# Performance work log

Hardware: AMD Instinct MI355X
Metric: run time of the kernel (lower is better)

The kernel has to match this reference:

```python
import jax, jax.numpy as jnp
import numpy as np

N = 1_000_000   # number of scattered items
D = 256         # in_embed_dim == key_proj_dim
E = 100_000     # nr_elements (number of segments)


def setup_inputs() -> dict:
    key = jax.random.key(0)
    k1, k2, k3, k4, k5 = jax.random.split(key, 5)
    bound = 1.0 / np.sqrt(D)
    scattered_values = jax.random.normal(k1, (N, D), dtype=jnp.float32)
    indices = jax.random.randint(k2, (N,), 0, E, dtype=jnp.int32)
    # key projection Linear(D, D) params (PyTorch default-style init)
    W_key = jax.random.uniform(k3, (D, D), minval=-bound, maxval=bound, dtype=jnp.float32)
    b_key = jax.random.uniform(k4, (D,), minval=-bound, maxval=bound, dtype=jnp.float32)
    # general_attention_weight ~ U(-1/sqrt(key_proj_dim), +)
    attn_w = jax.random.uniform(k5, (D,), minval=-bound, maxval=bound, dtype=jnp.float32)
    return {
        "scattered_values": scattered_values,
        "indices": indices,
        "nr_elements": E,
        "W_key": W_key,
        "b_key": b_key,
        "attn_w": attn_w,
    }


def reference(scattered_values, indices, nr_elements, W_key, b_key, attn_w):
    # key projection: [N, D]
    keys = scattered_values @ W_key.T + b_key
    # general attention logits, scaled: [N]
    probs = (keys @ attn_w) * (D ** -0.5)
    # scatter_softmax over segments (stable: subtract per-segment max)
    seg_max = jax.ops.segment_max(probs, indices, num_segments=nr_elements)
    seg_max = jnp.where(jnp.isfinite(seg_max), seg_max, 0.0)  # empty segments
    ex = jnp.exp(probs - seg_max[indices])
    denom = jax.ops.segment_sum(ex, indices, num_segments=nr_elements)
    scores = ex / denom[indices]
    # weighted scatter-sum of (unprojected) values: [E, D]
    attn_applied = jax.ops.segment_sum(
        scattered_values * scores[:, None], indices, num_segments=nr_elements
    )
    return scores, attn_applied
```

## Files before the change

kernel.cpp:

```cpp
#include <hip/hip_runtime.h>


#define DIM 256
#define WAVE 64

typedef float f4 __attribute__((ext_vector_type(4)));

__global__ void cw_rank_kernel(const float* __restrict__ W,
                               const float* __restrict__ b,
                               const float* __restrict__ a,
                               float* __restrict__ wc,
                               const int* __restrict__ idx,
                               int* __restrict__ counts,
                               int* __restrict__ rank, int n) {
    const int t = threadIdx.x;
    if (blockIdx.x <= DIM) {
        const int k = blockIdx.x;
        __shared__ float sm[256];
        sm[t] = (k < DIM) ? a[t] * W[t * DIM + k] : a[t] * b[t];
        __syncthreads();
        for (int d = 128; d; d >>= 1) {
            if (t < d) sm[t] += sm[t + d];
            __syncthreads();
        }
        if (t == 0) wc[k] = sm[0];
    } else {
        const int i = (blockIdx.x - DIM - 1) * 256 + t;
        if (i < n) rank[i] = atomicAdd(&counts[idx[i]], 1);
    }
}

__global__ void scan1_kernel(const int* __restrict__ counts,
                             int* __restrict__ offsets,
                             int* __restrict__ bsums, int e) {
    __shared__ int s[256];
    const int t = threadIdx.x, g = blockIdx.x * 256 + t;
    const int x = (g < e) ? counts[g] : 0;
    s[t] = x; __syncthreads();
    for (int d = 1; d < 256; d <<= 1) {
        const int v = (t >= d) ? s[t - d] : 0; __syncthreads();
        s[t] += v; __syncthreads();
    }
    if (g < e) offsets[g] = s[t] - x;
    if (t == 255) bsums[blockIdx.x] = s[255];
}

__global__ void scan2_kernel(int* __restrict__ bsums, int nb) {
    __shared__ int s[512];
    const int t = threadIdx.x;
    const int x = (t < nb) ? bsums[t] : 0;
    s[t] = x; __syncthreads();
    for (int d = 1; d < 512; d <<= 1) {
        const int v = (t >= d) ? s[t - d] : 0; __syncthreads();
        s[t] += v; __syncthreads();
    }
    if (t < nb) bsums[t] = s[t] - x;
}

__global__ void scan3_kernel(int* __restrict__ offsets,
                             const int* __restrict__ bsums, int e, int n) {
    const int g = blockIdx.x * 256 + threadIdx.x;
    if (g < e) offsets[g] += bsums[blockIdx.x];
    if (g == 0) offsets[e] = n;
}

__global__ void scatter_kernel(const int* __restrict__ idx,
                               const int* __restrict__ rank,
                               const int* __restrict__ offsets,
                               int* __restrict__ perm, int n) {
    const int i = blockIdx.x * 256 + threadIdx.x;
    if (i < n) perm[offsets[idx[i]] + rank[i]] = i;
}

__global__ void seg_fused_kernel(const f4* __restrict__ v4,
                                 const int* __restrict__ perm,
                                 const float* __restrict__ wc,
                                 const int* __restrict__ offsets,
                                 float* __restrict__ scores,
                                 float* __restrict__ attn, int e) {
    const int lane = threadIdx.x & (WAVE - 1);
    const int s = (blockIdx.x * blockDim.x + threadIdx.x) >> 6;
    if (s >= e) return;
    const f4 wf = ((const f4*)wc)[lane];
    const float c = wc[DIM];
    const int base = offsets[s];
    const int cnt  = offsets[s + 1] - base;
    f4 acc = {0.f, 0.f, 0.f, 0.f};

    if (cnt > 0 && cnt <= WAVE) {
        const int i_l = (lane < cnt) ? perm[base + lane] : 0;
        float myp = 0.f, d = 0.f;
        const int nch = (cnt + 7) >> 3;
        f4 cur[8], nxt[8];
        #pragma unroll
        for (int t = 0; t < 8; ++t)
            if (t < cnt)
                cur[t] = __builtin_nontemporal_load(
                    v4 + (size_t)__shfl(i_l, t, WAVE) * (DIM / 4) + lane);
        for (int ch = 0; ch < nch; ++ch) {
            const int st = ch * 8;
            if (ch + 1 < nch) {
                const int st2 = st + 8;
                #pragma unroll
                for (int t = 0; t < 8; ++t)
                    if (st2 + t < cnt)
                        nxt[t] = __builtin_nontemporal_load(
                            v4 + (size_t)__shfl(i_l, st2 + t, WAVE) * (DIM / 4) + lane);
            }
            #pragma unroll
            for (int t = 0; t < 8; ++t) {
                if (st + t < cnt) {
                    float pp = cur[t].x * wf.x + cur[t].y * wf.y
                             + cur[t].z * wf.z + cur[t].w * wf.w;
                    #pragma unroll
                    for (int off = 32; off; off >>= 1)
                        pp += __shfl_xor(pp, off, WAVE);
                    const float pe = __expf((pp + c) * 0.0625f);
                    d += pe;
                    acc.x += pe * cur[t].x; acc.y += pe * cur[t].y;
                    acc.z += pe * cur[t].z; acc.w += pe * cur[t].w;
                    if (lane == st + t) myp = pe;
                }
            }
            #pragma unroll
            for (int t = 0; t < 8; ++t) cur[t] = nxt[t];
        }
        const float inv = 1.f / d;
        if (lane < cnt) scores[i_l] = myp * inv;
        acc.x *= inv; acc.y *= inv; acc.z *= inv; acc.w *= inv;
    } else if (cnt > WAVE) {
        float d = 0.f;
        for (int t = 0; t < cnt; ++t) {
            const int i = perm[base + t];
            const f4 vv = v4[(size_t)i * (DIM / 4) + lane];
            float pp = vv.x * wf.x + vv.y * wf.y + vv.z * wf.z + vv.w * wf.w;
            #pragma unroll
            for (int off = 32; off; off >>= 1) pp += __shfl_xor(pp, off, WAVE);
            const float pe = __expf((pp + c) * 0.0625f);
            d += pe;
            acc.x += pe * vv.x; acc.y += pe * vv.y;
            acc.z += pe * vv.z; acc.w += pe * vv.w;
        }
        const float inv = 1.f / d;
        for (int t = 0; t < cnt; ++t) {
            const int i = perm[base + t];
            const f4 vv = v4[(size_t)i * (DIM / 4) + lane];
            float pp = vv.x * wf.x + vv.y * wf.y + vv.z * wf.z + vv.w * wf.w;
            #pragma unroll
            for (int off = 32; off; off >>= 1) pp += __shfl_xor(pp, off, WAVE);
            if (lane == 0) scores[i] = __expf((pp + c) * 0.0625f) * inv;
        }
        acc.x *= inv; acc.y *= inv; acc.z *= inv; acc.w *= inv;
    }
    __builtin_nontemporal_store(acc, (f4*)(attn + (size_t)s * DIM) + lane);
}

extern "C" void kernel_launch(void* const* d_in, const int* in_sizes, int n_in,
                              void* d_out, int out_size, void* d_ws, size_t ws_size,
                              hipStream_t stream) {
    const float* v   = (const float*)d_in[0];
    const int*   idx = (const int*)d_in[1];
    const float* W   = (const float*)d_in[3];
    const float* b   = (const float*)d_in[4];
    const float* a   = (const float*)d_in[5];

    const int n = in_sizes[0] / DIM;
    const int e = (out_size - n) / DIM;
    const int nb = (e + 255) / 256;

    float* scores = (float*)d_out;
    float* attn   = (float*)d_out + n;

    float* wc      = (float*)d_ws;
    int*   counts  = (int*)(wc + 512);
    int*   offsets = counts + e;
    int*   bsums   = offsets + e + 2;
    int*   rank    = bsums + 512;
    int*   perm    = rank + n;

    hipMemsetAsync(counts, 0, (size_t)e * sizeof(int), stream);
    cw_rank_kernel<<<DIM + 1 + (n + 255) / 256, 256, 0, stream>>>(
        W, b, a, wc, idx, counts, rank, n);
    scan1_kernel<<<nb, 256, 0, stream>>>(counts, offsets, bsums, e);
    scan2_kernel<<<1, 512, 0, stream>>>(bsums, nb);
    scan3_kernel<<<nb, 256, 0, stream>>>(offsets, bsums, e, n);
    scatter_kernel<<<(n + 255) / 256, 256, 0, stream>>>(idx, rank, offsets, perm, n);

    seg_fused_kernel<<<(e + 3) / 4, 256, 0, stream>>>((const f4*)v, perm, wc,
                                                      offsets, scores, attn, e);
}
```

Before: 284.1 us.

## Replace three-kernel scan with single-pass decoupled look-back scan

Merges the three prefix-scan kernels into one kernel. Each block publishes its aggregate and inclusive prefix through 64-bit status words and looks back at its predecessors using atomics. This removes two kernel launches and the global round trips through the block-sum buffer, so less time goes to launch overhead. In exchange it depends on blocks being scheduled roughly in order and can spin-wait. The status array is zeroed by extending the existing memset.

```diff
diff --git a/kernel.cpp b/kernel.cpp
--- a/kernel.cpp
+++ b/kernel.cpp
@@ -30,38 +30,45 @@
     }
 }
 
-__global__ void scan1_kernel(const int* __restrict__ counts,
-                             int* __restrict__ offsets,
-                             int* __restrict__ bsums, int e) {
+__global__ void scan_lb_kernel(const int* __restrict__ counts,
+                               int* __restrict__ offsets,
+                               unsigned long long* __restrict__ states,
+                               int e, int n) {
     __shared__ int s[256];
-    const int t = threadIdx.x, g = blockIdx.x * 256 + t;
+    __shared__ int px_sm;
+    const int c = blockIdx.x, t = threadIdx.x, g = c * 256 + t;
     const int x = (g < e) ? counts[g] : 0;
     s[t] = x; __syncthreads();
     for (int d = 1; d < 256; d <<= 1) {
         const int v = (t >= d) ? s[t - d] : 0; __syncthreads();
         s[t] += v; __syncthreads();
     }
-    if (g < e) offsets[g] = s[t] - x;
-    if (t == 255) bsums[blockIdx.x] = s[255];
-}
-
-__global__ void scan2_kernel(int* __restrict__ bsums, int nb) {
-    __shared__ int s[512];
-    const int t = threadIdx.x;
-    const int x = (t < nb) ? bsums[t] : 0;
-    s[t] = x; __syncthreads();
-    for (int d = 1; d < 512; d <<= 1) {
-        const int v = (t >= d) ? s[t - d] : 0; __syncthreads();
-        s[t] += v; __syncthreads();
+    const int A = s[255];
+    if (t == 0) {
+        int px = 0;
+        if (c == 0) {
+            __hip_atomic_store(&states[0], (2ULL << 32) | (unsigned)A,
+                               __ATOMIC_RELEASE, __HIP_MEMORY_SCOPE_AGENT);
+            offsets[e] = n;
+        } else {
+            __hip_atomic_store(&states[c], (1ULL << 32) | (unsigned)A,
+                               __ATOMIC_RELEASE, __HIP_MEMORY_SCOPE_AGENT);
+            for (int j = c - 1;;) {
+                const unsigned long long st = __hip_atomic_load(
+                    &states[j], __ATOMIC_ACQUIRE, __HIP_MEMORY_SCOPE_AGENT);
+                const unsigned stat = (unsigned)(st >> 32);
+                if (stat == 0u) continue;
+                px += (int)(unsigned)st;
+                if (stat == 2u) break;
+                --j;
+            }
+            __hip_atomic_store(&states[c], (2ULL << 32) | (unsigned)(px + A),
+                               __ATOMIC_RELEASE, __HIP_MEMORY_SCOPE_AGENT);
+        }
+        px_sm = px;
     }
-    if (t < nb) bsums[t] = s[t] - x;
-}
-
-__global__ void scan3_kernel(int* __restrict__ offsets,
-                             const int* __restrict__ bsums, int e, int n) {
-    const int g = blockIdx.x * 256 + threadIdx.x;
-    if (g < e) offsets[g] += bsums[blockIdx.x];
-    if (g == 0) offsets[e] = n;
+    __syncthreads();
+    if (g < e) offsets[g] = px_sm + s[t] - x;
 }
 
 __global__ void scatter_kernel(const int* __restrict__ idx,
@@ -171,19 +178,17 @@
     float* scores = (float*)d_out;
     float* attn   = (float*)d_out + n;
 
-    float* wc      = (float*)d_ws;
-    int*   counts  = (int*)(wc + 512);
-    int*   offsets = counts + e;
-    int*   bsums   = offsets + e + 2;
-    int*   rank    = bsums + 512;
+    float* wc     = (float*)d_ws;
+    int*   counts = (int*)(wc + 512);
+    unsigned long long* states = (unsigned long long*)(counts + e);
+    int*   offsets = (int*)(states + 512);
+    int*   rank    = offsets + e + 2;
     int*   perm    = rank + n;
 
-    hipMemsetAsync(counts, 0, (size_t)e * sizeof(int), stream);
+    hipMemsetAsync(counts, 0, (size_t)e * sizeof(int) + 512 * sizeof(unsigned long long), stream);
     cw_rank_kernel<<<DIM + 1 + (n + 255) / 256, 256, 0, stream>>>(
         W, b, a, wc, idx, counts, rank, n);
-    scan1_kernel<<<nb, 256, 0, stream>>>(counts, offsets, bsums, e);
-    scan2_kernel<<<1, 512, 0, stream>>>(bsums, nb);
-    scan3_kernel<<<nb, 256, 0, stream>>>(offsets, bsums, e, n);
+    scan_lb_kernel<<<nb, 256, 0, stream>>>(counts, offsets, states, e, n);
     scatter_kernel<<<(n + 255) / 256, 256, 0, stream>>>(idx, rank, offsets, perm, n);
 
     seg_fused_kernel<<<(e + 3) / 4, 256, 0, stream>>>((const f4*)v, perm, wc,
```

New measurement: 377.7 us. +32.9%, slower.
